# Kernel optimization log

Hardware: AMD Instinct MI355X
Metric: run time of the kernel (lower is better)

## Reference

```python
import jax, jax.numpy as jnp
import numpy as np

HEADS = 8
DIM_HEAD = 64
SCALE = DIM_HEAD ** -0.5


def setup_inputs() -> dict:
    key = jax.random.key(0)
    ks = jax.random.split(key, 7)
    b, p, n, dim = 4, 8, 512, 512
    inner = HEADS * DIM_HEAD
    std = dim ** -0.5
    return {
        "q_in": jax.random.normal(ks[0], (b, p, n, dim), jnp.float32),
        "kv_in": jax.random.normal(ks[1], (b, p, n, dim), jnp.float32),
        "Wq": jax.random.normal(ks[2], (dim, inner), jnp.float32) * std,
        "Wk": jax.random.normal(ks[3], (dim, inner), jnp.float32) * std,
        "Wv": jax.random.normal(ks[4], (dim, inner), jnp.float32) * std,
        "Wo": jax.random.normal(ks[5], (inner, dim), jnp.float32) * std,
        "bo": jnp.zeros((dim,), jnp.float32),
    }


def _split_heads(x):
    # [b, p, n, h*d] -> [b, h, p, n, d]
    b, p, n, hd = x.shape
    return x.reshape(b, p, n, HEADS, DIM_HEAD).transpose(0, 3, 1, 2, 4)


def reference(q_in, kv_in, Wq, Wk, Wv, Wo, bo):
    q = _split_heads(q_in @ Wq)
    k = _split_heads(kv_in @ Wk)
    v = _split_heads(kv_in @ Wv)
    dots = jnp.einsum('bhpid,bhpjd->bhpij', q, k) * SCALE
    attn = jax.nn.softmax(dots, axis=-1)
    out = jnp.einsum('bhpij,bhpjd->bhpid', attn, v)
    # [b, h, p, n, d] -> [b, p, n, h*d]
    b, h, p, n, d = out.shape
    out = out.transpose(0, 2, 3, 1, 4).reshape(b, p, n, h * d)
    return out @ Wo + bo
```

## Files before the change

### kernel.cpp

```cpp
#include <hip/hip_runtime.h>

typedef unsigned short u16;
typedef unsigned int   u32;
typedef u16  u16x8 __attribute__((ext_vector_type(8)));
typedef u16  u16x4 __attribute__((ext_vector_type(4)));
typedef float f32x4 __attribute__((ext_vector_type(4)));
typedef __bf16 bf16x8 __attribute__((ext_vector_type(8)));

#define SEQ   512
#define DIM   512
#define DHEAD 64
#define M_ROWS 16384

#define AS1 __attribute__((address_space(1)))
#define AS3 __attribute__((address_space(3)))
#define GLL16(gp, lp) __builtin_amdgcn_global_load_lds((const AS1 void*)(gp), (AS3 void*)(lp), 16, 0, 0)

__device__ __forceinline__ u16 f2b(float f) {
  u32 x = __builtin_bit_cast(u32, f);
  return (u16)((x + 0x7fffu + ((x >> 16) & 1u)) >> 16);
}

__global__ __launch_bounds__(256) void prep(const float* __restrict__ q,
                                            const float* __restrict__ kv,
                                            const float* __restrict__ Wq,
                                            const float* __restrict__ Wk,
                                            const float* __restrict__ Wv,
                                            const float* __restrict__ Wo,
                                            u16* __restrict__ qb,
                                            u16* __restrict__ kvb,
                                            u16* __restrict__ wout) {
  __shared__ float tile[32][33];
  const int bid = blockIdx.x;
  if (bid < 8192) {
    const float* src = (bid >= 4096) ? kv : q;
    u16* dst = (bid >= 4096) ? kvb : qb;
    size_t i = ((size_t)(bid & 4095) * 256 + threadIdx.x) * 8;
    float4 a = *reinterpret_cast<const float4*>(&src[i]);
    float4 b = *reinterpret_cast<const float4*>(&src[i + 4]);
    u16x8 o;
    o[0] = f2b(a.x); o[1] = f2b(a.y); o[2] = f2b(a.z); o[3] = f2b(a.w);
    o[4] = f2b(b.x); o[5] = f2b(b.y); o[6] = f2b(b.z); o[7] = f2b(b.w);
    *reinterpret_cast<u16x8*>(&dst[i]) = o;
  } else {
    const int rem = bid - 8192;
    const int z = rem >> 8;
    const int t = rem & 255;
    const int n0 = (t & 15) * 32;
    const int k0 = (t >> 4) * 32;
    const int tid = threadIdx.x;
    const int tx = tid & 31, ty = tid >> 5;
    const float* W = (z == 0) ? Wq : (z == 1) ? Wk : (z == 2) ? Wv : Wo;
#pragma unroll
    for (int i = 0; i < 4; i++) {
      int r = ty + i * 8;
      tile[r][tx] = W[(k0 + r) * DIM + n0 + tx];
    }
    __syncthreads();
    u16* o = wout + (size_t)z * DIM * DIM;
#pragma unroll
    for (int i = 0; i < 4; i++) {
      int r = ty + i * 8;
      o[(n0 + r) * DIM + k0 + tx] = f2b(tile[tx][r]);
    }
  }
}

__global__ __launch_bounds__(256, 2) void gemm_qkv(const u16* __restrict__ Qin,
                                                   const u16* __restrict__ KVin,
                                                   const u16* __restrict__ Wqt,
                                                   const u16* __restrict__ Wkt,
                                                   const u16* __restrict__ Wvt,
                                                   u16* __restrict__ Qb,
                                                   u16* __restrict__ Kb,
                                                   u16* __restrict__ Vt) {
  __shared__ __attribute__((aligned(16))) u16 As[256 * 32];
  __shared__ __attribute__((aligned(16))) u16 Bs[128 * 32];
  const int tid = threadIdx.x;
  const int lane = tid & 63;
  const int w = tid >> 6;
  const int l15 = lane & 15;
  const int quad = lane >> 4;
  const int z = blockIdx.z;
  const int bid = blockIdx.x;
  const int wr = (w >> 1) * 128, wc = (w & 1) * 64;
  const int srow = lane >> 2;
  const int scol = (lane & 3) * 8;

  int gm, gn;
  const u16 *A, *B;
  if (z < 2) {
    gm = (bid >> 2) * 256;  gn = (bid & 3) * 128;
    A = z ? KVin : Qin;  B = z ? Wkt : Wqt;
  } else {
    gm = (bid & 1) * 256;   gn = (bid >> 1) * 128;
    A = Wvt; B = KVin;
  }

  f32x4 acc[8][4] = {};

  for (int k0 = 0; k0 < DIM; k0 += 32) {
    __syncthreads();
#pragma unroll
    for (int i = 0; i < 4; i++) {
      int r0 = w * 64 + i * 16;
      GLL16(&A[(size_t)(gm + r0 + srow) * DIM + k0 + scol], &As[r0 * 32]);
    }
#pragma unroll
    for (int i = 0; i < 2; i++) {
      int r0 = w * 32 + i * 16;
      GLL16(&B[(size_t)(gn + r0 + srow) * DIM + k0 + scol], &Bs[r0 * 32]);
    }
    __syncthreads();

    bf16x8 af[8], bfr[4];
#pragma unroll
    for (int mt = 0; mt < 8; mt++)
      af[mt] = *reinterpret_cast<const bf16x8*>(&As[(wr + mt * 16 + l15) * 32 + quad * 8]);
#pragma unroll
    for (int nt = 0; nt < 4; nt++)
      bfr[nt] = *reinterpret_cast<const bf16x8*>(&Bs[(wc + nt * 16 + l15) * 32 + quad * 8]);
#pragma unroll
    for (int mt = 0; mt < 8; mt++)
#pragma unroll
      for (int nt = 0; nt < 4; nt++)
        acc[mt][nt] = __builtin_amdgcn_mfma_f32_16x16x32_bf16(af[mt], bfr[nt], acc[mt][nt], 0, 0, 0);
  }

  if (z < 2) {
    u16* C = (z == 0) ? Qb : Kb;
#pragma unroll
    for (int mt = 0; mt < 8; mt++)
#pragma unroll
      for (int nt = 0; nt < 4; nt++)
#pragma unroll
        for (int r = 0; r < 4; r++)
          C[(size_t)(gm + wr + mt * 16 + quad * 4 + r) * DIM + gn + wc + nt * 16 + l15] = f2b(acc[mt][nt][r]);
  } else {
#pragma unroll
    for (int mt = 0; mt < 8; mt++)
#pragma unroll
      for (int nt = 0; nt < 4; nt++)
#pragma unroll
        for (int r = 0; r < 4; r++)
          Vt[(size_t)(gm + wr + mt * 16 + quad * 4 + r) * M_ROWS + gn + wc + nt * 16 + l15] = f2b(acc[mt][nt][r]);
  }
}

__global__ __launch_bounds__(256) void attn(const u16* __restrict__ Qb,
                                            const u16* __restrict__ Kb,
                                            const u16* __restrict__ Vtg,
                                            u16* __restrict__ Ob) {
  __shared__ __attribute__((aligned(16))) u16 Ks[2 * 64 * 32];
  __shared__ __attribute__((aligned(16))) u16 Vs[2 * 64 * 32];
  __shared__ __attribute__((aligned(16))) u16 Pq[4][16 * 72];

  const int tid = threadIdx.x;
  const int lane = tid & 63;
  const int w = tid >> 6;
  const int l15 = lane & 15;
  const int quad = lane >> 4;
  const int srow = lane >> 2;
  const int scol = (lane & 3) * 8;

  const int d = blockIdx.x;
  const int bid = (d & 7) * 128 + (d >> 3);
  const int qt = bid & 3;
  const int bhp = bid >> 2;
  const int h = bhp & 7;
  const int bp = bhp >> 3;
  const int qrow0 = bp * SEQ + qt * 128;
  const int col0 = h * DHEAD;

  bf16x8 qf[2][2];
#pragma unroll
  for (int g = 0; g < 2; g++)
#pragma unroll
    for (int kd = 0; kd < 2; kd++)
      qf[g][kd] = *reinterpret_cast<const bf16x8*>(
          &Qb[(size_t)(qrow0 + w * 32 + g * 16 + l15) * DIM + col0 + kd * 32 + quad * 8]);

  float m_[2] = {-1e30f, -1e30f}, l_[2] = {0.0f, 0.0f};
  f32x4 o[2][4] = {};

  for (int j = 0; j < 8; j++) {
    __syncthreads();
    const int krow0 = bp * SEQ + j * 64;
#pragma unroll
    for (int i = 0; i < 2; i++) {
      int t = w * 2 + i;
      int plane = t & 1, chunk = t >> 1;
      GLL16(&Kb[(size_t)(krow0 + chunk * 16 + srow) * DIM + col0 + plane * 32 + scol],
            &Ks[plane * 2048 + chunk * 512]);
    }
#pragma unroll
    for (int i = 0; i < 2; i++) {
      int t = w * 2 + i;
      int plane = t & 1, chunk = t >> 1;
      GLL16(&Vtg[(size_t)(col0 + chunk * 16 + srow) * M_ROWS + krow0 + plane * 32 + scol],
            &Vs[plane * 2048 + chunk * 512]);
    }
    __syncthreads();

#pragma unroll
    for (int g = 0; g < 2; g++) {
      f32x4 st[4];
#pragma unroll
      for (int ct = 0; ct < 4; ct++) {
        f32x4 z = {};
#pragma unroll
        for (int kd = 0; kd < 2; kd++) {
          bf16x8 kf = *reinterpret_cast<const bf16x8*>(&Ks[kd * 2048 + (ct * 16 + l15) * 32 + quad * 8]);
          z = __builtin_amdgcn_mfma_f32_16x16x32_bf16(kf, qf[g][kd], z, 0, 0, 0);
        }
        st[ct] = z * 0.125f;
      }

      float pm = -1e30f;
#pragma unroll
      for (int ct = 0; ct < 4; ct++)
#pragma unroll
        for (int r = 0; r < 4; r++) pm = fmaxf(pm, st[ct][r]);
      pm = fmaxf(pm, __shfl_xor(pm, 16));
      pm = fmaxf(pm, __shfl_xor(pm, 32));
      float mn = fmaxf(m_[g], pm);
      float alpha = __expf(m_[g] - mn);
      m_[g] = mn;
      float rs = 0.0f;
#pragma unroll
      for (int ct = 0; ct < 4; ct++)
#pragma unroll
        for (int r = 0; r < 4; r++) {
          float pv = __expf(st[ct][r] - mn);
          st[ct][r] = pv;
          rs += pv;
        }
      rs += __shfl_xor(rs, 16);
      rs += __shfl_xor(rs, 32);
      l_[g] = l_[g] * alpha + rs;
#pragma unroll
      for (int r = 0; r < 4; r++) {
        float ar = __shfl(alpha, quad * 4 + r);
#pragma unroll
        for (int nt = 0; nt < 4; nt++) o[g][nt][r] *= ar;
      }

#pragma unroll
      for (int ct = 0; ct < 4; ct++) {
        u16x4 pk;
#pragma unroll
        for (int e = 0; e < 4; e++) pk[e] = f2b(st[ct][e]);
        *reinterpret_cast<u16x4*>(&Pq[w][l15 * 72 + ct * 16 + quad * 4]) = pk;
      }
      __threadfence_block();

#pragma unroll
      for (int c2 = 0; c2 < 2; c2++) {
        bf16x8 af = *reinterpret_cast<const bf16x8*>(&Pq[w][l15 * 72 + c2 * 32 + quad * 8]);
#pragma unroll
        for (int nt = 0; nt < 4; nt++) {
          bf16x8 bv = *reinterpret_cast<const bf16x8*>(&Vs[c2 * 2048 + (nt * 16 + l15) * 32 + quad * 8]);
          o[g][nt] = __builtin_amdgcn_mfma_f32_16x16x32_bf16(af, bv, o[g][nt], 0, 0, 0);
        }
      }
      __threadfence_block();
    }
  }

#pragma unroll
  for (int g = 0; g < 2; g++) {
    float inv = 1.0f / l_[g];
#pragma unroll
    for (int r = 0; r < 4; r++) {
      float lr = __shfl(inv, quad * 4 + r);
      int row = qrow0 + w * 32 + g * 16 + quad * 4 + r;
#pragma unroll
      for (int nt = 0; nt < 4; nt++)
        Ob[(size_t)row * DIM + col0 + nt * 16 + l15] = f2b(o[g][nt][r] * lr);
    }
  }
}

__global__ __launch_bounds__(256) void gemm_out(const u16* __restrict__ Ab,
                                                const u16* __restrict__ Bt,
                                                const float* __restrict__ bias,
                                                float* __restrict__ C) {
  __shared__ __attribute__((aligned(16))) u16 As[128 * 32];
  __shared__ __attribute__((aligned(16))) u16 Bs[128 * 32];
  const int tid = threadIdx.x;
  const int lane = tid & 63;
  const int w = tid >> 6;
  const int l15 = lane & 15;
  const int quad = lane >> 4;
  const int gm = blockIdx.y * 128;
  const int gn = blockIdx.x * 128;
  const int wr = (w >> 1) * 64, wc = (w & 1) * 64;
  const int srow = lane >> 2;
  const int scol = (lane & 3) * 8;

  f32x4 acc[4][4] = {};

  for (int k0 = 0; k0 < DIM; k0 += 32) {
    __syncthreads();
#pragma unroll
    for (int i = 0; i < 2; i++) {
      int r0 = w * 32 + i * 16;
      GLL16(&Ab[(size_t)(gm + r0 + srow) * DIM + k0 + scol], &As[r0 * 32]);
      GLL16(&Bt[(size_t)(gn + r0 + srow) * DIM + k0 + scol], &Bs[r0 * 32]);
    }
    __syncthreads();

    bf16x8 af[4], bfr[4];
#pragma unroll
    for (int mt = 0; mt < 4; mt++)
      af[mt] = *reinterpret_cast<const bf16x8*>(&As[(wr + mt * 16 + l15) * 32 + quad * 8]);
#pragma unroll
    for (int nt = 0; nt < 4; nt++)
      bfr[nt] = *reinterpret_cast<const bf16x8*>(&Bs[(wc + nt * 16 + l15) * 32 + quad * 8]);
#pragma unroll
    for (int mt = 0; mt < 4; mt++)
#pragma unroll
      for (int nt = 0; nt < 4; nt++)
        acc[mt][nt] = __builtin_amdgcn_mfma_f32_16x16x32_bf16(af[mt], bfr[nt], acc[mt][nt], 0, 0, 0);
  }

#pragma unroll
  for (int mt = 0; mt < 4; mt++)
#pragma unroll
    for (int nt = 0; nt < 4; nt++) {
      float bcol = bias[gn + wc + nt * 16 + l15];
#pragma unroll
      for (int r = 0; r < 4; r++)
        C[(size_t)(gm + wr + mt * 16 + quad * 4 + r) * DIM + gn + wc + nt * 16 + l15] = acc[mt][nt][r] + bcol;
    }
}

extern "C" void kernel_launch(void* const* d_in, const int* in_sizes, int n_in,
                              void* d_out, int out_size, void* d_ws, size_t ws_size,
                              hipStream_t stream) {
  const float* q_in  = (const float*)d_in[0];
  const float* kv_in = (const float*)d_in[1];
  const float* Wq    = (const float*)d_in[2];
  const float* Wk    = (const float*)d_in[3];
  const float* Wv    = (const float*)d_in[4];
  const float* Wo    = (const float*)d_in[5];
  const float* bo    = (const float*)d_in[6];
  float* out = (float*)d_out;

  u16* ws = (u16*)d_ws;
  u16* Wqt = ws;
  u16* Wkt = ws + 262144;
  u16* Wvt = ws + 524288;
  u16* Wot = ws + 786432;
  u16* Qb  = ws + 1048576;
  u16* Kb  = Qb + (size_t)M_ROWS * DIM;
  u16* Vtg = Kb + (size_t)M_ROWS * DIM;
  u16* Ob  = Vtg + (size_t)M_ROWS * DIM;
  u16* Qin_b  = (u16*)d_out;
  u16* KVin_b = Qin_b + (size_t)M_ROWS * DIM;

  prep<<<dim3(9216), 256, 0, stream>>>(q_in, kv_in, Wq, Wk, Wv, Wo, Qin_b, KVin_b, ws);
  gemm_qkv<<<dim3(256, 1, 3), 256, 0, stream>>>(Qin_b, KVin_b, Wqt, Wkt, Wvt, Qb, Kb, Vtg);
  attn<<<dim3(1024), 256, 0, stream>>>(Qb, Kb, Vtg, Ob);
  gemm_out<<<dim3(4, 128), 256, 0, stream>>>(Ob, Wot, bo, out);
}
```

Measured before the change: 228.5 us.

## Double-buffer LDS tiles with vmcnt waits in GEMM and attention kernels

Adds two-stage LDS buffers to the QKV GEMM, the attention kernel and the output GEMM. The next K-slice or KV tile is issued with global_load_lds before computing on the current one. Explicit s_waitcnt vmcnt plus s_barrier replaces the pair of __syncthreads per iteration, and the block fences become lgkmcnt waits. The aim is to hide global load latency behind MFMA work. The cost is doubled LDS use, which may lower occupancy, and reliance on hand-counted vmcnt values.

```diff
diff --git a/kernel.cpp b/kernel.cpp
--- a/kernel.cpp
+++ b/kernel.cpp
@@ -15,6 +15,10 @@
 #define AS1 __attribute__((address_space(1)))
 #define AS3 __attribute__((address_space(3)))
 #define GLL16(gp, lp) __builtin_amdgcn_global_load_lds((const AS1 void*)(gp), (AS3 void*)(lp), 16, 0, 0)
+
+#define WAIT_VM_BAR(LIT) do { asm volatile("s_waitcnt vmcnt(" LIT ")" ::: "memory"); __builtin_amdgcn_s_barrier(); } while (0)
+#define LGKM_BAR()       do { asm volatile("s_waitcnt lgkmcnt(0)" ::: "memory"); __builtin_amdgcn_s_barrier(); } while (0)
+#define LGKM_FENCE()     asm volatile("s_waitcnt lgkmcnt(0)" ::: "memory")
 
 __device__ __forceinline__ u16 f2b(float f) {
   u32 x = __builtin_bit_cast(u32, f);
@@ -74,8 +78,8 @@
                                                    u16* __restrict__ Qb,
                                                    u16* __restrict__ Kb,
                                                    u16* __restrict__ Vt) {
-  __shared__ __attribute__((aligned(16))) u16 As[256 * 32];
-  __shared__ __attribute__((aligned(16))) u16 Bs[128 * 32];
+  __shared__ __attribute__((aligned(16))) u16 As[2][256 * 32];
+  __shared__ __attribute__((aligned(16))) u16 Bs[2][128 * 32];
   const int tid = threadIdx.x;
   const int lane = tid & 63;
   const int w = tid >> 6;
@@ -99,32 +103,44 @@
 
   f32x4 acc[8][4] = {};
 
-  for (int k0 = 0; k0 < DIM; k0 += 32) {
-    __syncthreads();
+  auto stage = [&](int kk, int b) {
+    const int k0 = kk * 32;
 #pragma unroll
     for (int i = 0; i < 4; i++) {
       int r0 = w * 64 + i * 16;
-      GLL16(&A[(size_t)(gm + r0 + srow) * DIM + k0 + scol], &As[r0 * 32]);
+      GLL16(&A[(size_t)(gm + r0 + srow) * DIM + k0 + scol], &As[b][r0 * 32]);
     }
 #pragma unroll
     for (int i = 0; i < 2; i++) {
       int r0 = w * 32 + i * 16;
-      GLL16(&B[(size_t)(gn + r0 + srow) * DIM + k0 + scol], &Bs[r0 * 32]);
-    }
-    __syncthreads();
+      GLL16(&B[(size_t)(gn + r0 + srow) * DIM + k0 + scol], &Bs[b][r0 * 32]);
+    }
+  };
+
+  stage(0, 0);
+  for (int kk = 0; kk < 16; kk++) {
+    const int cur = kk & 1;
+    if (kk < 15) {
+      stage(kk + 1, cur ^ 1);
+      WAIT_VM_BAR("6");
+    } else {
+      WAIT_VM_BAR("0");
+    }
 
     bf16x8 af[8], bfr[4];
 #pragma unroll
     for (int mt = 0; mt < 8; mt++)
-      af[mt] = *reinterpret_cast<const bf16x8*>(&As[(wr + mt * 16 + l15) * 32 + quad * 8]);
+      af[mt] = *reinterpret_cast<const bf16x8*>(&As[cur][(wr + mt * 16 + l15) * 32 + quad * 8]);
 #pragma unroll
     for (int nt = 0; nt < 4; nt++)
-      bfr[nt] = *reinterpret_cast<const bf16x8*>(&Bs[(wc + nt * 16 + l15) * 32 + quad * 8]);
+      bfr[nt] = *reinterpret_cast<const bf16x8*>(&Bs[cur][(wc + nt * 16 + l15) * 32 + quad * 8]);
 #pragma unroll
     for (int mt = 0; mt < 8; mt++)
 #pragma unroll
       for (int nt = 0; nt < 4; nt++)
         acc[mt][nt] = __builtin_amdgcn_mfma_f32_16x16x32_bf16(af[mt], bfr[nt], acc[mt][nt], 0, 0, 0);
+
+    LGKM_BAR();
   }
 
   if (z < 2) {
@@ -151,8 +167,8 @@
                                             const u16* __restrict__ Kb,
                                             const u16* __restrict__ Vtg,
                                             u16* __restrict__ Ob) {
-  __shared__ __attribute__((aligned(16))) u16 Ks[2 * 64 * 32];
-  __shared__ __attribute__((aligned(16))) u16 Vs[2 * 64 * 32];
+  __shared__ __attribute__((aligned(16))) u16 Ks[2][2 * 64 * 32];
+  __shared__ __attribute__((aligned(16))) u16 Vs[2][2 * 64 * 32];
   __shared__ __attribute__((aligned(16))) u16 Pq[4][16 * 72];
 
   const int tid = threadIdx.x;
@@ -183,24 +199,33 @@
   float m_[2] = {-1e30f, -1e30f}, l_[2] = {0.0f, 0.0f};
   f32x4 o[2][4] = {};
 
-  for (int j = 0; j < 8; j++) {
-    __syncthreads();
-    const int krow0 = bp * SEQ + j * 64;
+  auto stageKV = [&](int jj, int b) {
+    const int kr0 = bp * SEQ + jj * 64;
 #pragma unroll
     for (int i = 0; i < 2; i++) {
       int t = w * 2 + i;
       int plane = t & 1, chunk = t >> 1;
-      GLL16(&Kb[(size_t)(krow0 + chunk * 16 + srow) * DIM + col0 + plane * 32 + scol],
-            &Ks[plane * 2048 + chunk * 512]);
+      GLL16(&Kb[(size_t)(kr0 + chunk * 16 + srow) * DIM + col0 + plane * 32 + scol],
+            &Ks[b][plane * 2048 + chunk * 512]);
     }
 #pragma unroll
     for (int i = 0; i < 2; i++) {
       int t = w * 2 + i;
       int plane = t & 1, chunk = t >> 1;
-      GLL16(&Vtg[(size_t)(col0 + chunk * 16 + srow) * M_ROWS + krow0 + plane * 32 + scol],
-            &Vs[plane * 2048 + chunk * 512]);
-    }
-    __syncthreads();
+      GLL16(&Vtg[(size_t)(col0 + chunk * 16 + srow) * M_ROWS + kr0 + plane * 32 + scol],
+            &Vs[b][plane * 2048 + chunk * 512]);
+    }
+  };
+
+  stageKV(0, 0);
+  for (int j = 0; j < 8; j++) {
+    const int cur = j & 1;
+    if (j < 7) {
+      stageKV(j + 1, cur ^ 1);
+      WAIT_VM_BAR("4");
+    } else {
+      WAIT_VM_BAR("0");
+    }
 
 #pragma unroll
     for (int g = 0; g < 2; g++) {
@@ -210,7 +235,7 @@
         f32x4 z = {};
 #pragma unroll
         for (int kd = 0; kd < 2; kd++) {
-          bf16x8 kf = *reinterpret_cast<const bf16x8*>(&Ks[kd * 2048 + (ct * 16 + l15) * 32 + quad * 8]);
+          bf16x8 kf = *reinterpret_cast<const bf16x8*>(&Ks[cur][kd * 2048 + (ct * 16 + l15) * 32 + quad * 8]);
           z = __builtin_amdgcn_mfma_f32_16x16x32_bf16(kf, qf[g][kd], z, 0, 0, 0);
         }
         st[ct] = z * 0.125f;
@@ -252,19 +277,21 @@
         for (int e = 0; e < 4; e++) pk[e] = f2b(st[ct][e]);
         *reinterpret_cast<u16x4*>(&Pq[w][l15 * 72 + ct * 16 + quad * 4]) = pk;
       }
-      __threadfence_block();
+      LGKM_FENCE();
 
 #pragma unroll
       for (int c2 = 0; c2 < 2; c2++) {
         bf16x8 af = *reinterpret_cast<const bf16x8*>(&Pq[w][l15 * 72 + c2 * 32 + quad * 8]);
 #pragma unroll
         for (int nt = 0; nt < 4; nt++) {
-          bf16x8 bv = *reinterpret_cast<const bf16x8*>(&Vs[c2 * 2048 + (nt * 16 + l15) * 32 + quad * 8]);
+          bf16x8 bv = *reinterpret_cast<const bf16x8*>(&Vs[cur][c2 * 2048 + (nt * 16 + l15) * 32 + quad * 8]);
           o[g][nt] = __builtin_amdgcn_mfma_f32_16x16x32_bf16(af, bv, o[g][nt], 0, 0, 0);
         }
       }
-      __threadfence_block();
-    }
+      LGKM_FENCE();
+    }
+
+    LGKM_BAR();
   }
 
 #pragma unroll
@@ -285,8 +312,8 @@
                                                 const u16* __restrict__ Bt,
                                                 const float* __restrict__ bias,
                                                 float* __restrict__ C) {
-  __shared__ __attribute__((aligned(16))) u16 As[128 * 32];
-  __shared__ __attribute__((aligned(16))) u16 Bs[128 * 32];
+  __shared__ __attribute__((aligned(16))) u16 As[2][128 * 32];
+  __shared__ __attribute__((aligned(16))) u16 Bs[2][128 * 32];
   const int tid = threadIdx.x;
   const int lane = tid & 63;
   const int w = tid >> 6;
@@ -300,28 +327,40 @@
 
   f32x4 acc[4][4] = {};
 
-  for (int k0 = 0; k0 < DIM; k0 += 32) {
-    __syncthreads();
+  auto stage = [&](int kk, int b) {
+    const int k0 = kk * 32;
 #pragma unroll
     for (int i = 0; i < 2; i++) {
       int r0 = w * 32 + i * 16;
-      GLL16(&Ab[(size_t)(gm + r0 + srow) * DIM + k0 + scol], &As[r0 * 32]);
-      GLL16(&Bt[(size_t)(gn + r0 + srow) * DIM + k0 + scol], &Bs[r0 * 32]);
-    }
-    __syncthreads();
+      GLL16(&Ab[(size_t)(gm + r0 + srow) * DIM + k0 + scol], &As[b][r0 * 32]);
+      GLL16(&Bt[(size_t)(gn + r0 + srow) * DIM + k0 + scol], &Bs[b][r0 * 32]);
+    }
+  };
+
+  stage(0, 0);
+  for (int kk = 0; kk < 16; kk++) {
+    const int cur = kk & 1;
+    if (kk < 15) {
+      stage(kk + 1, cur ^ 1);
+      WAIT_VM_BAR("4");
+    } else {
+      WAIT_VM_BAR("0");
+    }
 
     bf16x8 af[4], bfr[4];
 #pragma unroll
     for (int mt = 0; mt < 4; mt++)
-      af[mt] = *reinterpret_cast<const bf16x8*>(&As[(wr + mt * 16 + l15) * 32 + quad * 8]);
+      af[mt] = *reinterpret_cast<const bf16x8*>(&As[cur][(wr + mt * 16 + l15) * 32 + quad * 8]);
 #pragma unroll
     for (int nt = 0; nt < 4; nt++)
-      bfr[nt] = *reinterpret_cast<const bf16x8*>(&Bs[(wc + nt * 16 + l15) * 32 + quad * 8]);
+      bfr[nt] = *reinterpret_cast<const bf16x8*>(&Bs[cur][(wc + nt * 16 + l15) * 32 + quad * 8]);
 #pragma unroll
     for (int mt = 0; mt < 4; mt++)
 #pragma unroll
       for (int nt = 0; nt < 4; nt++)
         acc[mt][nt] = __builtin_amdgcn_mfma_f32_16x16x32_bf16(af[mt], bfr[nt], acc[mt][nt], 0, 0, 0);
+
+    LGKM_BAR();
   }
 
 #pragma unroll
```

Measured after the change: 224.7 us. About the same (-1.7%).
